# Kernel tuning notes

Measured on AMD Instinct MI355X. Metric: run time of the kernel, lower is better.

The kernel has to match this reference:

```python
import jax, jax.numpy as jnp
import numpy as np

EPS = 1e-5

def setup_inputs() -> dict:
    key = jax.random.key(0)
    k1, k2 = jax.random.split(key)
    B, S, F = 16, 8192, 256
    x = jax.random.normal(k1, (B, S, F), dtype=jnp.float32)
    change_points = (jax.random.uniform(k2, (B, S)) < 0.001).astype(jnp.int32)
    affine_weight = jnp.ones((F,), dtype=jnp.float32)
    affine_bias = jnp.zeros((F,), dtype=jnp.float32)
    return {"x": x, "affine_weight": affine_weight, "affine_bias": affine_bias,
            "change_points": change_points}


def _segment_normalize(x, affine_weight, affine_bias, change_points):
    # x: [B, S, F]; change_points: [B, S] int
    B, S, F = x.shape
    # Torch loop: a boundary fires at position i (i >= 1) if ANY batch has a cp.
    ind = (jnp.sum(change_points, axis=0) > 0).astype(jnp.int32)  # [S]
    ind = ind.at[0].set(0)  # loop starts at i=1; position 0 never splits
    seg_id = jnp.cumsum(ind)  # [S], segment index shared across batch

    xt = jnp.swapaxes(x, 0, 1)  # [S, B, F]
    ones = jnp.ones((S,), dtype=x.dtype)
    counts = jax.ops.segment_sum(ones, seg_id, num_segments=S)  # [S]
    ssum = jax.ops.segment_sum(xt, seg_id, num_segments=S)      # [S, B, F]
    ssq = jax.ops.segment_sum(xt * xt, seg_id, num_segments=S)  # [S, B, F]
    cnt = jnp.maximum(counts, 1.0)[:, None, None]
    mean = ssum / cnt                                   # per-segment mean (biased var)
    var = jnp.maximum(ssq / cnt - mean * mean, 0.0)
    std = jnp.sqrt(var + EPS)
    # stats are .detach()ed in the original
    mean_t = jax.lax.stop_gradient(mean)[seg_id]  # gather back to [S, B, F]
    std_t = jax.lax.stop_gradient(std)[seg_id]
    xn = (xt - mean_t) / std_t
    xn = jnp.swapaxes(xn, 0, 1)  # [B, S, F]
    xn = xn * affine_weight + affine_bias
    return xn


def reference(x, affine_weight, affine_bias, change_points):
    return _segment_normalize(x, affine_weight, affine_bias, change_points)
```

## Files before the change

kernel.cpp:

```cpp
#include <hip/hip_runtime.h>

#define BSZ 16
#define SSZ 8192
#define F4  64
#define EPSV 1e-5f
#define SEGCAP 256
#define NBLK 2048

typedef float f32x4 __attribute__((ext_vector_type(4)));

__global__ void cp_reduce_kernel(const int* __restrict__ cp, int* __restrict__ ind) {
    int s = blockIdx.x * blockDim.x + threadIdx.x;
    if (s >= SSZ) return;
    int a = 0;
#pragma unroll
    for (int b = 0; b < BSZ; ++b) a |= cp[b * SSZ + s];
    ind[s] = (s == 0) ? 0 : (a != 0 ? 1 : 0);
}

__global__ __launch_bounds__(1024) void scan_sort_kernel(const int* __restrict__ ind,
                                                         int* __restrict__ sorted_st,
                                                         int* __restrict__ sorted_en,
                                                         int* __restrict__ meta) {
    __shared__ int lds[1024];
    __shared__ int sstart[SEGCAP];
    __shared__ int snseg;
    const int t = threadIdx.x;
    int vals[8];
    int tot = 0;
#pragma unroll
    for (int i = 0; i < 8; ++i) { int v = ind[t * 8 + i]; vals[i] = v; tot += v; }
    lds[t] = tot;
    __syncthreads();
    for (int off = 1; off < 1024; off <<= 1) {
        int a = lds[t];
        int b = (t >= off) ? lds[t - off] : 0;
        __syncthreads();
        lds[t] = a + b;
        __syncthreads();
    }
    int run = lds[t] - tot;
#pragma unroll
    for (int i = 0; i < 8; ++i) {
        run += vals[i];
        if (vals[i] && run < SEGCAP) sstart[run] = t * 8 + i;
    }
    if (t == 0) sstart[0] = 0;
    if (t == 1023) { int n = lds[1023] + 1; snseg = n < SEGCAP ? n : SEGCAP; }
    __syncthreads();

    const int nseg = snseg;
    if (t < nseg) {
        const int st = sstart[t];
        const int en = (t + 1 < nseg) ? sstart[t + 1] : SSZ;
        const int len = en - st;
        int rank = 0;
        for (int j = 0; j < nseg; ++j) {
            const int stj = sstart[j];
            const int enj = (j + 1 < nseg) ? sstart[j + 1] : SSZ;
            const int lj = enj - stj;
            rank += (lj > len) || (lj == len && j < t);
        }
        sorted_st[rank] = st;
        sorted_en[rank] = en;
    }
    if (t == 0) meta[0] = nseg;
}

__global__ __launch_bounds__(256) void segnorm_kernel(const f32x4* __restrict__ x4,
                                                      const f32x4* __restrict__ w4p,
                                                      const f32x4* __restrict__ b4p,
                                                      const int* __restrict__ sorted_st,
                                                      const int* __restrict__ sorted_en,
                                                      const int* __restrict__ meta,
                                                      f32x4* __restrict__ out4) {
    __shared__ f32x4 lsum[8][32];
    __shared__ f32x4 lssq[8][32];
    __shared__ f32x4 lmean[32];
    __shared__ f32x4 lrstd[32];
    const int nitems = meta[0] * 32;
    const int col = threadIdx.x & 31;
    const int rg = threadIdx.x >> 5;

    for (int item = blockIdx.x; item < nitems; item += NBLK) {
        const int k = item >> 5;
        const int b = (item >> 1) & 15;
        const int fh = item & 1;
        const int st = sorted_st[k];
        const int en = sorted_en[k];
        const f32x4* px = x4 + (size_t)b * SSZ * F4 + fh * 32 + col;

        f32x4 sum = {0.f, 0.f, 0.f, 0.f};
        f32x4 ssq = {0.f, 0.f, 0.f, 0.f};
        for (int s = st + rg; s < en; s += 8) {
            f32x4 v = px[(size_t)s * F4];
            sum += v;
            ssq += v * v;
        }
        lsum[rg][col] = sum;
        lssq[rg][col] = ssq;
        __syncthreads();
        if (threadIdx.x < 32) {
            f32x4 S = {0.f, 0.f, 0.f, 0.f};
            f32x4 Q = {0.f, 0.f, 0.f, 0.f};
#pragma unroll
            for (int r = 0; r < 8; ++r) { S += lsum[r][threadIdx.x]; Q += lssq[r][threadIdx.x]; }
            const float rc = 1.0f / (float)(en - st);
            f32x4 m = S * rc;
            f32x4 var = Q * rc - m * m;
            f32x4 rr;
            rr.x = 1.0f / sqrtf(fmaxf(var.x, 0.f) + EPSV);
            rr.y = 1.0f / sqrtf(fmaxf(var.y, 0.f) + EPSV);
            rr.z = 1.0f / sqrtf(fmaxf(var.z, 0.f) + EPSV);
            rr.w = 1.0f / sqrtf(fmaxf(var.w, 0.f) + EPSV);
            lmean[threadIdx.x] = m;
            lrstd[threadIdx.x] = rr;
        }
        __syncthreads();
        const f32x4 m = lmean[col];
        const f32x4 r = lrstd[col];
        const f32x4 w = w4p[fh * 32 + col];
        const f32x4 bb = b4p[fh * 32 + col];
        f32x4* po = out4 + (size_t)b * SSZ * F4 + fh * 32 + col;
        for (int s = st + rg; s < en; s += 8) {
            f32x4 v = px[(size_t)s * F4];
            f32x4 o = (v - m) * r * w + bb;
            __builtin_nontemporal_store(o, &po[(size_t)s * F4]);
        }
    }
}

extern "C" void kernel_launch(void* const* d_in, const int* in_sizes, int n_in,
                              void* d_out, int out_size, void* d_ws, size_t ws_size,
                              hipStream_t stream) {
    const f32x4* x = (const f32x4*)d_in[0];
    const f32x4* w = (const f32x4*)d_in[1];
    const f32x4* bias = (const f32x4*)d_in[2];
    const int* cp = (const int*)d_in[3];

    char* ws = (char*)d_ws;
    int* meta = (int*)ws;
    int* sorted_st = (int*)(ws + 1024);
    int* sorted_en = (int*)(ws + 4096);
    int* ind = (int*)(ws + 8192);

    cp_reduce_kernel<<<(SSZ + 255) / 256, 256, 0, stream>>>(cp, ind);
    scan_sort_kernel<<<1, 1024, 0, stream>>>(ind, sorted_st, sorted_en, meta);
    segnorm_kernel<<<NBLK, 256, 0, stream>>>(x, w, bias, sorted_st, sorted_en, meta,
                                             (f32x4*)d_out);
}
```

Before: 100.6 us.

## Split segment statistics into chunked partial-reduction kernel before normalization pass

```diff
diff --git a/kernel.cpp b/kernel.cpp
--- a/kernel.cpp
+++ b/kernel.cpp
@@ -5,6 +5,8 @@
 #define F4  64
 #define EPSV 1e-5f
 #define SEGCAP 256
+#define CHCAP  384
+#define CH 64
 #define NBLK 2048
 
 typedef float f32x4 __attribute__((ext_vector_type(4)));
@@ -19,52 +21,133 @@
 }
 
 __global__ __launch_bounds__(1024) void scan_sort_kernel(const int* __restrict__ ind,
+                                                         int* __restrict__ seg_starts,
+                                                         int* __restrict__ chunk_base,
+                                                         int* __restrict__ chunk_seg,
                                                          int* __restrict__ sorted_st,
                                                          int* __restrict__ sorted_en,
+                                                         int* __restrict__ sorted_c0,
+                                                         int* __restrict__ sorted_c1,
                                                          int* __restrict__ meta) {
-    __shared__ int lds[1024];
+    __shared__ int ldsi[1024];
     __shared__ int sstart[SEGCAP];
+    __shared__ int lcb[SEGCAP + 1];
     __shared__ int snseg;
     const int t = threadIdx.x;
     int vals[8];
     int tot = 0;
 #pragma unroll
     for (int i = 0; i < 8; ++i) { int v = ind[t * 8 + i]; vals[i] = v; tot += v; }
-    lds[t] = tot;
+    ldsi[t] = tot;
     __syncthreads();
     for (int off = 1; off < 1024; off <<= 1) {
-        int a = lds[t];
-        int b = (t >= off) ? lds[t - off] : 0;
-        __syncthreads();
-        lds[t] = a + b;
-        __syncthreads();
-    }
-    int run = lds[t] - tot;
+        int a = ldsi[t];
+        int b = (t >= off) ? ldsi[t - off] : 0;
+        __syncthreads();
+        ldsi[t] = a + b;
+        __syncthreads();
+    }
+    int run = ldsi[t] - tot;
 #pragma unroll
     for (int i = 0; i < 8; ++i) {
         run += vals[i];
         if (vals[i] && run < SEGCAP) sstart[run] = t * 8 + i;
     }
     if (t == 0) sstart[0] = 0;
-    if (t == 1023) { int n = lds[1023] + 1; snseg = n < SEGCAP ? n : SEGCAP; }
+    if (t == 1023) { int n = ldsi[1023] + 1; snseg = n < SEGCAP ? n : SEGCAP; }
     __syncthreads();
 
     const int nseg = snseg;
+    if (t < nseg) seg_starts[t] = sstart[t];
+
+    int nch = 0;
+    if (t < nseg) {
+        int st = sstart[t];
+        int en = (t + 1 < nseg) ? sstart[t + 1] : SSZ;
+        nch = (en - st + CH - 1) / CH;
+    }
+    ldsi[t] = nch;
+    __syncthreads();
+    for (int off = 1; off < 1024; off <<= 1) {
+        int a = ldsi[t];
+        int b = (t >= off) ? ldsi[t - off] : 0;
+        __syncthreads();
+        ldsi[t] = a + b;
+        __syncthreads();
+    }
+    int cbase = ldsi[t] - nch;
+    if (t < nseg) {
+        chunk_base[t] = cbase;
+        lcb[t] = cbase;
+        for (int j = 0; j < nch; ++j) chunk_seg[cbase + j] = t;
+    }
+    if (t == 1023) {
+        lcb[nseg] = ldsi[1023];
+        meta[0] = nseg;
+        meta[1] = ldsi[1023] * BSZ;
+        meta[2] = nseg * BSZ * 2;
+    }
+    __syncthreads();
+
     if (t < nseg) {
         const int st = sstart[t];
         const int en = (t + 1 < nseg) ? sstart[t + 1] : SSZ;
         const int len = en - st;
         int rank = 0;
         for (int j = 0; j < nseg; ++j) {
-            const int stj = sstart[j];
-            const int enj = (j + 1 < nseg) ? sstart[j + 1] : SSZ;
-            const int lj = enj - stj;
+            const int lj = ((j + 1 < nseg) ? sstart[j + 1] : SSZ) - sstart[j];
             rank += (lj > len) || (lj == len && j < t);
         }
         sorted_st[rank] = st;
         sorted_en[rank] = en;
-    }
-    if (t == 0) meta[0] = nseg;
+        sorted_c0[rank] = lcb[t];
+        sorted_c1[rank] = lcb[t + 1];
+    }
+}
+
+__global__ __launch_bounds__(256) void stats_kernel(const f32x4* __restrict__ x4,
+                                                    const int* __restrict__ seg_starts,
+                                                    const int* __restrict__ chunk_base,
+                                                    const int* __restrict__ chunk_seg,
+                                                    const int* __restrict__ meta,
+                                                    f32x4* __restrict__ psum,
+                                                    f32x4* __restrict__ pssq) {
+    __shared__ f32x4 lsum[4][64];
+    __shared__ f32x4 lssq[4][64];
+    const int nitems = meta[1];
+    const int nseg = meta[0];
+    const int lane = threadIdx.x & 63;
+    const int wave = threadIdx.x >> 6;
+    for (int item = blockIdx.x; item < nitems; item += gridDim.x) {
+        const int c = item >> 4;
+        const int b = item & 15;
+        const int seg = chunk_seg[c];
+        const int j = c - chunk_base[seg];
+        const int st = seg_starts[seg];
+        const int en = (seg + 1 < nseg) ? seg_starts[seg + 1] : SSZ;
+        const int s0 = st + j * CH;
+        const int s1 = min(en, s0 + CH);
+        const f32x4* px = x4 + (size_t)b * SSZ * F4 + lane;
+
+        f32x4 sum = {0.f, 0.f, 0.f, 0.f};
+        f32x4 ssq = {0.f, 0.f, 0.f, 0.f};
+        for (int s = s0 + wave; s < s1; s += 4) {
+            f32x4 v = px[(size_t)s * F4];
+            sum += v;
+            ssq += v * v;
+        }
+        lsum[wave][lane] = sum;
+        lssq[wave][lane] = ssq;
+        __syncthreads();
+        if (wave == 0) {
+            f32x4 o = lsum[0][lane] + lsum[1][lane] + lsum[2][lane] + lsum[3][lane];
+            __builtin_nontemporal_store(o, &psum[((size_t)c * BSZ + b) * F4 + lane]);
+        } else if (wave == 1) {
+            f32x4 o = lssq[0][lane] + lssq[1][lane] + lssq[2][lane] + lssq[3][lane];
+            __builtin_nontemporal_store(o, &pssq[((size_t)c * BSZ + b) * F4 + lane]);
+        }
+        __syncthreads();
+    }
 }
 
 __global__ __launch_bounds__(256) void segnorm_kernel(const f32x4* __restrict__ x4,
@@ -72,13 +155,13 @@
                                                       const f32x4* __restrict__ b4p,
                                                       const int* __restrict__ sorted_st,
                                                       const int* __restrict__ sorted_en,
+                                                      const int* __restrict__ sorted_c0,
+                                                      const int* __restrict__ sorted_c1,
                                                       const int* __restrict__ meta,
+                                                      const f32x4* __restrict__ psum,
+                                                      const f32x4* __restrict__ pssq,
                                                       f32x4* __restrict__ out4) {
-    __shared__ f32x4 lsum[8][32];
-    __shared__ f32x4 lssq[8][32];
-    __shared__ f32x4 lmean[32];
-    __shared__ f32x4 lrstd[32];
-    const int nitems = meta[0] * 32;
+    const int nitems = meta[2];
     const int col = threadIdx.x & 31;
     const int rg = threadIdx.x >> 5;
 
@@ -88,40 +171,29 @@
         const int fh = item & 1;
         const int st = sorted_st[k];
         const int en = sorted_en[k];
-        const f32x4* px = x4 + (size_t)b * SSZ * F4 + fh * 32 + col;
-
-        f32x4 sum = {0.f, 0.f, 0.f, 0.f};
-        f32x4 ssq = {0.f, 0.f, 0.f, 0.f};
-        for (int s = st + rg; s < en; s += 8) {
-            f32x4 v = px[(size_t)s * F4];
-            sum += v;
-            ssq += v * v;
-        }
-        lsum[rg][col] = sum;
-        lssq[rg][col] = ssq;
-        __syncthreads();
-        if (threadIdx.x < 32) {
-            f32x4 S = {0.f, 0.f, 0.f, 0.f};
-            f32x4 Q = {0.f, 0.f, 0.f, 0.f};
-#pragma unroll
-            for (int r = 0; r < 8; ++r) { S += lsum[r][threadIdx.x]; Q += lssq[r][threadIdx.x]; }
-            const float rc = 1.0f / (float)(en - st);
-            f32x4 m = S * rc;
-            f32x4 var = Q * rc - m * m;
-            f32x4 rr;
-            rr.x = 1.0f / sqrtf(fmaxf(var.x, 0.f) + EPSV);
-            rr.y = 1.0f / sqrtf(fmaxf(var.y, 0.f) + EPSV);
-            rr.z = 1.0f / sqrtf(fmaxf(var.z, 0.f) + EPSV);
-            rr.w = 1.0f / sqrtf(fmaxf(var.w, 0.f) + EPSV);
-            lmean[threadIdx.x] = m;
-            lrstd[threadIdx.x] = rr;
-        }
-        __syncthreads();
-        const f32x4 m = lmean[col];
-        const f32x4 r = lrstd[col];
-        const f32x4 w = w4p[fh * 32 + col];
-        const f32x4 bb = b4p[fh * 32 + col];
-        f32x4* po = out4 + (size_t)b * SSZ * F4 + fh * 32 + col;
+        const int c0 = sorted_c0[k];
+        const int c1 = sorted_c1[k];
+        const int fc = fh * 32 + col;
+
+        f32x4 S = {0.f, 0.f, 0.f, 0.f};
+        f32x4 Q = {0.f, 0.f, 0.f, 0.f};
+        for (int c = c0; c < c1; ++c) {
+            S += psum[((size_t)c * BSZ + b) * F4 + fc];
+            Q += pssq[((size_t)c * BSZ + b) * F4 + fc];
+        }
+        const float rc = 1.0f / (float)(en - st);
+        const f32x4 m = S * rc;
+        f32x4 var = Q * rc - m * m;
+        f32x4 r;
+        r.x = 1.0f / sqrtf(fmaxf(var.x, 0.f) + EPSV);
+        r.y = 1.0f / sqrtf(fmaxf(var.y, 0.f) + EPSV);
+        r.z = 1.0f / sqrtf(fmaxf(var.z, 0.f) + EPSV);
+        r.w = 1.0f / sqrtf(fmaxf(var.w, 0.f) + EPSV);
+        const f32x4 w = w4p[fc];
+        const f32x4 bb = b4p[fc];
+
+        const f32x4* px = x4 + (size_t)b * SSZ * F4 + fc;
+        f32x4* po = out4 + (size_t)b * SSZ * F4 + fc;
         for (int s = st + rg; s < en; s += 8) {
             f32x4 v = px[(size_t)s * F4];
             f32x4 o = (v - m) * r * w + bb;
@@ -140,12 +212,24 @@
 
     char* ws = (char*)d_ws;
     int* meta = (int*)ws;
-    int* sorted_st = (int*)(ws + 1024);
-    int* sorted_en = (int*)(ws + 4096);
-    int* ind = (int*)(ws + 8192);
+    int* seg_starts = (int*)(ws + 1024);
+    int* chunk_base = (int*)(ws + 2048);
+    int* chunk_seg = (int*)(ws + 4096);
+    int* sorted_st = (int*)(ws + 8192);
+    int* sorted_en = (int*)(ws + 10240);
+    int* sorted_c0 = (int*)(ws + 12288);
+    int* sorted_c1 = (int*)(ws + 14336);
+    int* ind = (int*)(ws + 16384);
+    f32x4* psum = (f32x4*)(ws + 65536);
+    f32x4* pssq = psum + (size_t)CHCAP * BSZ * F4;
 
     cp_reduce_kernel<<<(SSZ + 255) / 256, 256, 0, stream>>>(cp, ind);
-    scan_sort_kernel<<<1, 1024, 0, stream>>>(ind, sorted_st, sorted_en, meta);
-    segnorm_kernel<<<NBLK, 256, 0, stream>>>(x, w, bias, sorted_st, sorted_en, meta,
+    scan_sort_kernel<<<1, 1024, 0, stream>>>(ind, seg_starts, chunk_base, chunk_seg,
+                                             sorted_st, sorted_en, sorted_c0, sorted_c1,
+                                             meta);
+    stats_kernel<<<4096, 256, 0, stream>>>(x, seg_starts, chunk_base, chunk_seg, meta,
+                                           psum, pssq);
+    segnorm_kernel<<<NBLK, 256, 0, stream>>>(x, w, bias, sorted_st, sorted_en,
+                                             sorted_c0, sorted_c1, meta, psum, pssq,
                                              (f32x4*)d_out);
 }
```

Result: slower. 103.6 us (+3.0%).
